# Optimization experiments

Hardware: AMD Instinct MI355X
Metric: run time of the kernel (lower is better)

Reference implementation:

```python
import jax, jax.numpy as jnp
import numpy as np

NEG_SLOPE = 0.01  # torch LeakyReLU default


def gru_layer(x, w_ih, w_hh, b_ih, b_hh):
    # x: [T, B, in], weights per torch.nn.GRU convention: [3H, in]/[3H, H], gates (r,z,n)
    H = w_hh.shape[1]
    def step(h, x_t):
        gi = x_t @ w_ih.T + b_ih            # [B, 3H]
        gh = h @ w_hh.T + b_hh              # [B, 3H]
        i_r, i_z, i_n = jnp.split(gi, 3, axis=-1)
        h_r, h_z, h_n = jnp.split(gh, 3, axis=-1)
        r = jax.nn.sigmoid(i_r + h_r)
        z = jax.nn.sigmoid(i_z + h_z)
        n = jnp.tanh(i_n + r * h_n)
        h_new = (1.0 - z) * n + z * h
        return h_new, h_new
    h0 = jnp.zeros((x.shape[1], H), x.dtype)
    _, ys = jax.lax.scan(step, h0, x)
    return ys  # [T, B, H]


def setup_inputs() -> dict:
    key = jax.random.key(0)
    ks = jax.random.split(key, 16)
    T, B, V, H, L2 = 128, 2048, 64, 256, 100
    s = 1.0 / np.sqrt(H)
    d = {
        'tokens': jax.random.randint(ks[0], (T, B), 0, V, dtype=jnp.int32),
        'lens': jax.random.randint(ks[1], (B,), 0, T, dtype=jnp.int32),
        'emb': jax.random.normal(ks[2], (V, H), jnp.float32),
        'w_ih0': jax.random.normal(ks[3], (3 * H, H), jnp.float32) * s,
        'w_hh0': jax.random.normal(ks[4], (3 * H, H), jnp.float32) * s,
        'b_ih0': jax.random.normal(ks[5], (3 * H,), jnp.float32) * s,
        'b_hh0': jax.random.normal(ks[6], (3 * H,), jnp.float32) * s,
        'w_ih1': jax.random.normal(ks[7], (3 * H, H), jnp.float32) * s,
        'w_hh1': jax.random.normal(ks[8], (3 * H, H), jnp.float32) * s,
        'b_ih1': jax.random.normal(ks[9], (3 * H,), jnp.float32) * s,
        'b_hh1': jax.random.normal(ks[10], (3 * H,), jnp.float32) * s,
        'w1': jax.random.normal(ks[11], (H, H), jnp.float32) * s,
        'b1': jax.random.normal(ks[12], (H,), jnp.float32) * s,
        'w2': jax.random.normal(ks[13], (L2, H), jnp.float32) * s,
        'b2': jax.random.normal(ks[14], (L2,), jnp.float32) * s,
    }
    return d


def reference(tokens, lens, emb, w_ih0, w_hh0, b_ih0, b_hh0,
              w_ih1, w_hh1, b_ih1, b_hh1, w1, b1, w2, b2):
    x = emb[tokens]                                   # [T, B, H] embedding lookup
    h1 = gru_layer(x, w_ih0, w_hh0, b_ih0, b_hh0)     # layer 0
    h2 = gru_layer(h1, w_ih1, w_hh1, b_ih1, b_hh1)    # layer 1
    B = tokens.shape[1]
    out_t = h2[lens, jnp.arange(B)]                   # [B, H] gather per-example timestep
    z = out_t @ w1.T + b1
    z = jnp.where(z >= 0, z, NEG_SLOPE * z)           # LeakyReLU
    enc = z @ w2.T + b2                               # [B, 2*latent]
    return enc
```

## Files before the change

### kernel.cpp

```cpp
#include <hip/hip_runtime.h>
#include <hip/hip_bf16.h>

typedef __attribute__((ext_vector_type(8))) short bh8;
typedef __attribute__((ext_vector_type(4))) short sh4;
typedef __attribute__((ext_vector_type(4))) float f4;

static constexpr int T_STEPS = 128;
static constexpr int BTOT    = 2048;
static constexpr int HD      = 256;
static constexpr int NG      = 768;
static constexpr int LOUT    = 100;

__device__ __forceinline__ short f2bf(float f){
  unsigned u = __builtin_bit_cast(unsigned, f);
  unsigned r = (u + 0x7FFFu + ((u >> 16) & 1u)) >> 16;
  return (short)(unsigned short)r;
}
__device__ __forceinline__ float bf2f(short s){
  unsigned u = ((unsigned)(unsigned short)s) << 16;
  return __builtin_bit_cast(float, u);
}
__device__ __forceinline__ f4 mfma16(bh8 a, bh8 b, f4 c){
  return __builtin_amdgcn_mfma_f32_16x16x32_bf16(a, b, c, 0, 0, 0);
}
__device__ __forceinline__ float sigm(float x){
  return __builtin_amdgcn_rcpf(1.f + __expf(-x));
}
__device__ __forceinline__ float tanh_f(float x){
  return 1.f - 2.f*__builtin_amdgcn_rcpf(1.f + __expf(2.f*x));
}

__global__ void e0g_kernel(const float* __restrict__ emb, const float* __restrict__ w_ih0,
                           const float* __restrict__ b_ih0, const float* __restrict__ b_hh0,
                           short* __restrict__ E0g)
{
  int tid = blockIdx.x*blockDim.x + threadIdx.x;
  if (tid >= 64*NG) return;
  int v = tid / NG, n = tid % NG;
  const float4* er = (const float4*)(emb + (size_t)v*HD);
  const float4* wr = (const float4*)(w_ih0 + (size_t)n*HD);
  float s = 0.f;
#pragma unroll 4
  for (int k=0;k<HD/4;++k){
    float4 a = er[k], b = wr[k];
    s += a.x*b.x + a.y*b.y + a.z*b.z + a.w*b.w;
  }
  s += b_ih0[n];
  if (n < 512) s += b_hh0[n];
  int g = n >> 8, j = n & 255;
  int wid = j >> 5, c = (j >> 4) & 1, l15 = j & 15;
  E0g[(size_t)v*1024 + wid*128 + l15*8 + g*2 + c] = f2bf(s);
}

__global__ void pack_kernel(const float* __restrict__ w_hh0, const float* __restrict__ w_ih1,
                            const float* __restrict__ w_hh1, const float* __restrict__ w1,
                            const float* __restrict__ w2, short* __restrict__ pack)
{
  int tid = blockIdx.x*blockDim.x + threadIdx.x;
  if (tid >= 1336*64) return;
  int t = tid >> 6, lane = tid & 63;
  int l15 = lane & 15, lq = lane >> 4;
  const float* src = nullptr;
  bool zero = false;
  if (t < 1152){
    int m = t/384, tt = t%384, ct = tt/8, kt = tt%8;
    int n = ct*16 + l15;
    const float* Wm = (m==0) ? w_hh0 : (m==1 ? w_ih1 : w_hh1);
    src = Wm + (size_t)n*HD + kt*32 + lq*8;
  } else if (t < 1280){
    int tt = t - 1152, w = tt/16, rem = tt%16, ntt = rem/8, kt = rem%8;
    int n = w*32 + ntt*16 + l15;
    src = w1 + (size_t)n*HD + kt*32 + lq*8;
  } else {
    int tt = t - 1280, ntt = tt/8, kt = tt%8;
    int n = ntt*16 + l15;
    if (n < LOUT) src = w2 + (size_t)n*HD + kt*32 + lq*8;
    else zero = true;
  }
  bh8 o;
#pragma unroll
  for (int e=0;e<8;++e) o[e] = zero ? (short)0 : f2bf(src[e]);
  ((bh8*)pack)[tid] = o;
}


__device__ __forceinline__ void layer0_body(
    int bid, const int* __restrict__ tokens, const short* __restrict__ E0g,
    const short* __restrict__ pack, const float* __restrict__ b_hh0,
    short* __restrict__ s0c, short* __restrict__ h0g, int tc, int Tc,
    short (&st)[2][16*264])
{
  const int tid = threadIdx.x;
  const int wid = tid >> 6;
  const int lane = tid & 63;
  const int l15 = lane & 15, lq = lane >> 4;
  const int b0 = bid * 16;

  bh8 W[3][2][8];
  {
    const bh8* pt = (const bh8*)pack;
#pragma unroll
    for (int g=0;g<3;++g)
#pragma unroll
      for (int c=0;c<2;++c)
#pragma unroll
        for (int kt=0;kt<8;++kt)
          W[g][c][kt] = pt[(size_t)((g*16 + wid*2 + c)*8 + kt)*64 + lane];
  }
  float bhn0[2];
#pragma unroll
  for (int c=0;c<2;++c) bhn0[c] = b_hh0[512 + wid*32 + c*16 + l15];

  if (tc == 0){
    for (int i=tid;i<16*264;i+=512) st[0][i] = 0;
  } else {
    for (int i=tid;i<16*256;i+=512)
      st[0][(i>>8)*264 + (i&255)] = h0g[(size_t)(b0 + (i>>8))*HD + (i&255)];
  }

  const int e0base = wid*128 + l15*8;
  bh8 ev[4];
  {
    const int tg0 = tc*Tc;
    int tokr[4];
#pragma unroll
    for (int r=0;r<4;++r) tokr[r] = tokens[(size_t)tg0*BTOT + b0 + lq*4 + r];
#pragma unroll
    for (int r=0;r<4;++r)
      ev[r] = *(const bh8*)(E0g + (size_t)tokr[r]*1024 + e0base);
  }
  __syncthreads();

  const f4 zf = {0.f,0.f,0.f,0.f};
  const int crow = tid >> 5, ccol8 = (tid & 31)*8;

#pragma unroll 1
  for (int t=0; t<Tc; ++t){
    const int p = t & 1;
    const int tg = tc*Tc + t;
    const int tn = (tg+1 < T_STEPS) ? tg+1 : T_STEPS-1;
    int tokn[4];
#pragma unroll
    for (int r=0;r<4;++r) tokn[r] = tokens[(size_t)tn*BTOT + b0 + lq*4 + r];
    f4 acc[3][2];
#pragma unroll
    for (int g=0;g<3;++g){ acc[g][0]=zf; acc[g][1]=zf; }
    {
      const short* sp = &st[p][l15*264 + lq*8];
#pragma unroll
      for (int kt=0;kt<8;++kt){
        bh8 a = *(const bh8*)(sp + kt*32);
#pragma unroll
        for (int g=0;g<3;++g){
          acc[g][0] = mfma16(a, W[g][0][kt], acc[g][0]);
          acc[g][1] = mfma16(a, W[g][1][kt], acc[g][1]);
        }
      }
    }
    if (t > 0){
      bh8 cv = *(const bh8*)(&st[p][crow*264 + ccol8]);
      *(bh8*)(s0c + ((size_t)(t-1)*BTOT + b0 + crow)*HD + ccol8) = cv;
    }
    {
      short* stw = st[p^1];
#pragma unroll
      for (int c=0;c<2;++c){
        const int jh = wid*32 + c*16 + l15;
#pragma unroll
        for (int r4=0;r4<4;++r4){
          const int row = lq*4 + r4;
          const float er = bf2f(ev[r4][c]);
          const float ez = bf2f(ev[r4][2+c]);
          const float en = bf2f(ev[r4][4+c]);
          const float rg = sigm(acc[0][c][r4] + er);
          const float zg = sigm(acc[1][c][r4] + ez);
          const float ng = tanh_f(en + rg*(acc[2][c][r4] + bhn0[c]));
          const float ho = bf2f(st[p][row*264 + jh]);
          const float h = ng + zg*(ho - ng);
          stw[row*264 + jh] = f2bf(h);
        }
      }
    }
#pragma unroll
    for (int r=0;r<4;++r)
      ev[r] = *(const bh8*)(E0g + (size_t)tokn[r]*1024 + e0base);
    __syncthreads();
  }
  {
    bh8 cv = *(const bh8*)(&st[Tc & 1][crow*264 + ccol8]);
    *(bh8*)(s0c + ((size_t)(Tc-1)*BTOT + b0 + crow)*HD + ccol8) = cv;
    *(bh8*)(h0g + ((size_t)(b0 + crow))*HD + ccol8) = cv;
  }
}

__device__ __forceinline__ void layer1_body(
    int bid, const int* __restrict__ lens, const short* __restrict__ gi1p,
    const short* __restrict__ pack, const float* __restrict__ b_hh1,
    short* __restrict__ h1g, short* __restrict__ outbuf, int tc, int Tc,
    short (&st)[2][16*264])
{
  const int tid = threadIdx.x;
  const int wid = tid >> 6;
  const int lane = tid & 63;
  const int l15 = lane & 15, lq = lane >> 4;
  const int b0 = bid * 16;
  const int bblk = bid;

  bh8 W[3][2][8];
  {
    const bh8* pt = (const bh8*)pack;
#pragma unroll
    for (int g=0;g<3;++g)
#pragma unroll
      for (int c=0;c<2;++c)
#pragma unroll
        for (int kt=0;kt<8;++kt)
          W[g][c][kt] = pt[(size_t)(768 + (g*16 + wid*2 + c)*8 + kt)*64 + lane];
  }
  float bhn1[2];
#pragma unroll
  for (int c=0;c<2;++c) bhn1[c] = b_hh1[512 + wid*32 + c*16 + l15];

  int mylens[4];
#pragma unroll
  for (int r=0;r<4;++r) mylens[r] = lens[b0 + lq*4 + r];

  if (tc == 0){
    for (int i=tid;i<16*264;i+=512) st[0][i] = 0;
  } else {
    for (int i=tid;i<16*256;i+=512)
      st[0][(i>>8)*264 + (i&255)] = h1g[(size_t)(b0 + (i>>8))*HD + (i&255)];
  }

  bh8 gv[3];
#pragma unroll
  for (int g=0;g<3;++g)
    gv[g] = *(const bh8*)(gi1p + ((size_t)bblk*512 + tid)*24 + g*8);
  __syncthreads();

  const f4 zf = {0.f,0.f,0.f,0.f};
  const int crow = tid >> 5, ccol8 = (tid & 31)*8;

#pragma unroll 1
  for (int t=0; t<Tc; ++t){
    const int p = t & 1;
    const int tg = tc*Tc + t;
    f4 acc[3][2];
#pragma unroll
    for (int g=0;g<3;++g){ acc[g][0]=zf; acc[g][1]=zf; }
    {
      const short* sp = &st[p][l15*264 + lq*8];
#pragma unroll
      for (int kt=0;kt<8;++kt){
        bh8 a = *(const bh8*)(sp + kt*32);
#pragma unroll
        for (int g=0;g<3;++g){
          acc[g][0] = mfma16(a, W[g][0][kt], acc[g][0]);
          acc[g][1] = mfma16(a, W[g][1][kt], acc[g][1]);
        }
      }
    }
    {
      short* stw = st[p^1];
#pragma unroll
      for (int c=0;c<2;++c){
        const int jh = wid*32 + c*16 + l15;
#pragma unroll
        for (int r4=0;r4<4;++r4){
          const int row = lq*4 + r4;
          const float gr = bf2f(gv[0][c*4+r4]);
          const float gz = bf2f(gv[1][c*4+r4]);
          const float gn = bf2f(gv[2][c*4+r4]);
          const float rg = sigm(acc[0][c][r4] + gr);
          const float zg = sigm(acc[1][c][r4] + gz);
          const float ng = tanh_f(gn + rg*(acc[2][c][r4] + bhn1[c]));
          const float ho = bf2f(st[p][row*264 + jh]);
          const float h = ng + zg*(ho - ng);
          const short hb = f2bf(h);
          stw[row*264 + jh] = hb;
          if (tg == mylens[r4]) outbuf[(size_t)(b0 + row)*HD + jh] = hb;
        }
      }
    }
    if (t+1 < Tc){
#pragma unroll
      for (int g=0;g<3;++g)
        gv[g] = *(const bh8*)(gi1p + (((size_t)(t+1)*128 + bblk)*512 + tid)*24 + g*8);
    }
    __syncthreads();
  }
  {
    bh8 cv = *(const bh8*)(&st[Tc & 1][crow*264 + ccol8]);
    *(bh8*)(h1g + ((size_t)(b0 + crow))*HD + ccol8) = cv;
  }
}

__global__ __launch_bounds__(512, 1)
void scan_fat(const int* __restrict__ tokens, const short* __restrict__ E0g,
              const short* __restrict__ pack, const float* __restrict__ b_hh0,
              short* __restrict__ s0c, short* __restrict__ h0g,
              const int* __restrict__ lens, const short* __restrict__ gi1p,
              const float* __restrict__ b_hh1, short* __restrict__ h1g,
              short* __restrict__ outbuf, int tc0, int tc1, int Tc)
{
  __shared__ __align__(16) short st[2][16*264];
  const int bx = blockIdx.x;
  if (bx < 128){
    if (tc0 >= 0)
      layer0_body(bx, tokens, E0g, pack, b_hh0, s0c, h0g, tc0, Tc, st);
  } else {
    if (tc1 >= 0)
      layer1_body(bx - 128, lens, gi1p, pack, b_hh1, h1g, outbuf, tc1, Tc, st);
  }
}

__global__ __launch_bounds__(256, 1)
void gi1_gemm(const short* __restrict__ s0c, const short* __restrict__ pack,
              const float* __restrict__ b_ih1, const float* __restrict__ b_hh1,
              short* __restrict__ gi1p, int NC)
{
  const int tid = threadIdx.x;
  const int wid = tid >> 6;
  const int lane = tid & 63;
  const int l15 = lane & 15, lq = lane >> 4;

  __shared__ __align__(16) short ab[2][16*264];
  __shared__ float bi[NG];
  for (int i=tid;i<NG;i+=256) bi[i] = b_ih1[i] + ((i < 512) ? b_hh1[i] : 0.f);

  bh8 W[12][8];
#pragma unroll
  for (int i=0;i<12;++i)
#pragma unroll
    for (int kt=0;kt<8;++kt)
      W[i][kt] = ((const bh8*)pack)[(size_t)(384 + (wid*12+i)*8 + kt)*64 + lane];

  int ci = blockIdx.x;
  if (ci >= NC) return;
  bh8 sr[2];
#pragma unroll
  for (int j=0;j<2;++j){
    int q = tid + j*256;
    sr[j] = *(const bh8*)(s0c + (size_t)ci*4096 + q*8);
  }
#pragma unroll
  for (int j=0;j<2;++j){
    int q = tid + j*256, row = q>>5, col8 = (q&31)*8;
    *(bh8*)(&ab[0][row*264 + col8]) = sr[j];
  }
  __syncthreads();

  const f4 zf = {0.f,0.f,0.f,0.f};
  int p = 0;
#pragma unroll 1
  for (; ci < NC; ci += gridDim.x){
    const int cin = ci + (int)gridDim.x;
    const bool more = (cin < NC);
    if (more){
#pragma unroll
      for (int j=0;j<2;++j){
        int q = tid + j*256;
        sr[j] = *(const bh8*)(s0c + (size_t)cin*4096 + q*8);
      }
    }
    f4 acc[12];
#pragma unroll
    for (int i=0;i<12;++i) acc[i] = zf;
    const short* sp = &ab[p][l15*264 + lq*8];
#pragma unroll
    for (int kt=0;kt<8;++kt){
      bh8 a = *(const bh8*)(sp + kt*32);
#pragma unroll
      for (int i=0;i<12;++i) acc[i] = mfma16(a, W[i][kt], acc[i]);
    }
#pragma unroll
    for (int i=0;i<12;++i){
      const int gc = (wid*12+i)*16 + l15;
      const int g = gc >> 8, j = gc & 255;
      const int widp = j >> 5, c = (j >> 4) & 1;
      const int tidp = widp*64 + lq*16 + l15;
      const float b = bi[gc];
      sh4 v;
#pragma unroll
      for (int r4=0;r4<4;++r4) v[r4] = f2bf(acc[i][r4] + b);
      *(sh4*)(gi1p + ((size_t)ci*512 + tidp)*24 + g*8 + c*4) = v;
    }
    if (more){
#pragma unroll
      for (int j=0;j<2;++j){
        int q = tid + j*256, row = q>>5, col8 = (q&31)*8;
        *(bh8*)(&ab[p^1][row*264 + col8]) = sr[j];
      }
    }
    p ^= 1;
    __syncthreads();
  }
}

__global__ __launch_bounds__(512, 1)
void head_kernel(const short* __restrict__ outbuf, const short* __restrict__ pack,
                 const float* __restrict__ b1, const float* __restrict__ b2,
                 float* __restrict__ out)
{
  const int tid = threadIdx.x;
  const int wid = tid >> 6;
  const int lane = tid & 63;
  const int l15 = lane & 15, lq = lane >> 4;
  const int b0 = blockIdx.x * 32;

  __shared__ __align__(16) short zA[32*264];
  __shared__ __align__(16) short zB[32*264];
  __shared__ float b1s[HD], b2s[112];
  if (tid < HD)  b1s[tid] = b1[tid];
  if (tid < 112) b2s[tid] = (tid < LOUT) ? b2[tid] : 0.f;

  for (int i=tid;i<32*256;i+=512){
    int row = i >> 8, col = i & 255;
    zA[row*264 + col] = outbuf[(size_t)(b0 + row)*HD + col];
  }
  __syncthreads();

  const f4 zf = {0.f,0.f,0.f,0.f};
  const int afrag = l15*264 + lq*8;
  constexpr int RT1 = 16*264;
  const bh8* packW1 = (const bh8*)pack + (size_t)(1152 + wid*16)*64 + lane;
  const bh8* packW2 = (const bh8*)pack + (size_t)(1280 + wid*8 )*64 + lane;

  {
    f4 az[2][2]; az[0][0]=zf; az[0][1]=zf; az[1][0]=zf; az[1][1]=zf;
#pragma unroll
    for (int kt=0;kt<8;++kt){
      bh8 a0 = *(const bh8*)(&zA[afrag + kt*32]);
      bh8 a1 = *(const bh8*)(&zA[afrag + RT1 + kt*32]);
#pragma unroll
      for (int nt=0;nt<2;++nt){
        bh8 b = packW1[(nt*8+kt)*64];
        az[nt][0] = mfma16(a0, b, az[nt][0]);
        az[nt][1] = mfma16(a1, b, az[nt][1]);
      }
    }
#pragma unroll
    for (int rt=0;rt<2;++rt)
#pragma unroll
      for (int nt=0;nt<2;++nt){
        const int jb = wid*32 + nt*16 + l15;
#pragma unroll
        for (int r4=0;r4<4;++r4){
          float v = az[nt][rt][r4] + b1s[jb];
          v = (v >= 0.f) ? v : 0.01f*v;
          zB[(rt*16+lq*4+r4)*264 + jb] = f2bf(v);
        }
      }
  }
  __syncthreads();

  if (wid < 7){
    f4 acc2[2]; acc2[0]=zf; acc2[1]=zf;
#pragma unroll
    for (int kt=0;kt<8;++kt){
      bh8 a0 = *(const bh8*)(&zB[afrag + kt*32]);
      bh8 a1 = *(const bh8*)(&zB[afrag + RT1 + kt*32]);
      bh8 b = packW2[kt*64];
      acc2[0] = mfma16(a0, b, acc2[0]);
      acc2[1] = mfma16(a1, b, acc2[1]);
    }
    const int n2 = wid*16 + l15;
    if (n2 < LOUT){
#pragma unroll
      for (int rt=0;rt<2;++rt)
#pragma unroll
        for (int r4=0;r4<4;++r4)
          out[(size_t)(b0 + rt*16 + lq*4 + r4)*LOUT + n2] = acc2[rt][r4] + b2s[n2];
    }
  }
}

extern "C" void kernel_launch(void* const* d_in, const int* in_sizes, int n_in,
                              void* d_out, int out_size, void* d_ws, size_t ws_size,
                              hipStream_t stream)
{
  const int*   tokens = (const int*)  d_in[0];
  const int*   lens   = (const int*)  d_in[1];
  const float* emb    = (const float*)d_in[2];
  const float* w_ih0  = (const float*)d_in[3];
  const float* w_hh0  = (const float*)d_in[4];
  const float* b_ih0  = (const float*)d_in[5];
  const float* b_hh0  = (const float*)d_in[6];
  const float* w_ih1  = (const float*)d_in[7];
  const float* w_hh1  = (const float*)d_in[8];
  const float* b_ih1  = (const float*)d_in[9];
  const float* b_hh1  = (const float*)d_in[10];
  const float* w1     = (const float*)d_in[11];
  const float* b1     = (const float*)d_in[12];
  const float* w2     = (const float*)d_in[13];
  const float* b2     = (const float*)d_in[14];

  char* ws = (char*)d_ws;
  size_t off = 0;
  short* pack = (short*)(ws + off); off += (size_t)1336*1024;
  short* E0g  = (short*)(ws + off); off += (size_t)64*1024*2;
  short* h0g  = (short*)(ws + off); off += (size_t)BTOT*HD*2;
  short* h1g  = (short*)(ws + off); off += (size_t)BTOT*HD*2;
  short* outb = (short*)(ws + off); off += (size_t)BTOT*HD*2;
  const size_t fixed = off;
  const size_t perT = (size_t)BTOT*HD*2 + (size_t)BTOT*NG*2;
  int Tc = T_STEPS;
  while (Tc > 1 && fixed + (size_t)Tc*perT > ws_size) Tc >>= 1;
  short* s0c  = (short*)(ws + fixed);
  short* gi1p = (short*)(ws + fixed + (size_t)Tc*BTOT*HD*2);

  e0g_kernel <<<(64*NG + 255)/256,   256, 0, stream>>>(emb, w_ih0, b_ih0, b_hh0, E0g);
  pack_kernel<<<(1336*64 + 255)/256, 256, 0, stream>>>(w_hh0, w_ih1, w_hh1, w1, w2, pack);

  const int nch = T_STEPS / Tc;
  for (int k = 0; k <= nch; ++k){
    const int tc0 = (k < nch) ? k : -1;
    const int tc1 = k - 1;
    scan_fat<<<256, 512, 0, stream>>>(tokens, E0g, pack, b_hh0, s0c, h0g,
                                      lens, gi1p, b_hh1, h1g, outb, tc0, tc1, Tc);
    if (k < nch)
      gi1_gemm<<<256, 256, 0, stream>>>(s0c, pack, b_ih1, b_hh1, gi1p, Tc*BTOT/16);
  }
  head_kernel<<<BTOT/32, 512, 0, stream>>>(outb, pack, b1, b2, (float*)d_out);
}
```

Before: 675.7 us.

## Keep GRU hidden state in fp32 registers, widen gi1 GEMM, cap chunk length

The layer-0 and layer-1 scans now keep the previous hidden value for each lane's outputs in fp32 registers instead of reading it back from the bf16 LDS tile. This removes an LDS read per element and avoids compounding bf16 rounding in the recurrence. The gi1 GEMM moves to 512 threads with 6 gate tiles per wave instead of 12, and precomputes bias and output offsets in registers, which cuts per-thread register pressure. The time chunk is capped at 32 steps, so the pipelined layer-0 / GEMM / layer-1 schedule has more stages, at the cost of more kernel launches.

```diff
diff --git a/kernel.cpp b/kernel.cpp
--- a/kernel.cpp
+++ b/kernel.cpp
@@ -111,9 +111,19 @@
 #pragma unroll
   for (int c=0;c<2;++c) bhn0[c] = b_hh0[512 + wid*32 + c*16 + l15];
 
+  float h0s[2][4];
   if (tc == 0){
+#pragma unroll
+    for (int c=0;c<2;++c)
+#pragma unroll
+      for (int r=0;r<4;++r) h0s[c][r] = 0.f;
     for (int i=tid;i<16*264;i+=512) st[0][i] = 0;
   } else {
+#pragma unroll
+    for (int c=0;c<2;++c)
+#pragma unroll
+      for (int r=0;r<4;++r)
+        h0s[c][r] = bf2f(h0g[(size_t)(b0 + lq*4 + r)*HD + wid*32 + c*16 + l15]);
     for (int i=tid;i<16*256;i+=512)
       st[0][(i>>8)*264 + (i&255)] = h0g[(size_t)(b0 + (i>>8))*HD + (i&255)];
   }
@@ -175,8 +185,8 @@
           const float rg = sigm(acc[0][c][r4] + er);
           const float zg = sigm(acc[1][c][r4] + ez);
           const float ng = tanh_f(en + rg*(acc[2][c][r4] + bhn0[c]));
-          const float ho = bf2f(st[p][row*264 + jh]);
-          const float h = ng + zg*(ho - ng);
+          const float h = ng + zg*(h0s[c][r4] - ng);
+          h0s[c][r4] = h;
           stw[row*264 + jh] = f2bf(h);
         }
       }
@@ -225,9 +235,19 @@
 #pragma unroll
   for (int r=0;r<4;++r) mylens[r] = lens[b0 + lq*4 + r];
 
+  float h1s[2][4];
   if (tc == 0){
+#pragma unroll
+    for (int c=0;c<2;++c)
+#pragma unroll
+      for (int r=0;r<4;++r) h1s[c][r] = 0.f;
     for (int i=tid;i<16*264;i+=512) st[0][i] = 0;
   } else {
+#pragma unroll
+    for (int c=0;c<2;++c)
+#pragma unroll
+      for (int r=0;r<4;++r)
+        h1s[c][r] = bf2f(h1g[(size_t)(b0 + lq*4 + r)*HD + wid*32 + c*16 + l15]);
     for (int i=tid;i<16*256;i+=512)
       st[0][(i>>8)*264 + (i&255)] = h1g[(size_t)(b0 + (i>>8))*HD + (i&255)];
   }
@@ -274,8 +294,8 @@
           const float rg = sigm(acc[0][c][r4] + gr);
           const float zg = sigm(acc[1][c][r4] + gz);
           const float ng = tanh_f(gn + rg*(acc[2][c][r4] + bhn1[c]));
-          const float ho = bf2f(st[p][row*264 + jh]);
-          const float h = ng + zg*(ho - ng);
+          const float h = ng + zg*(h1s[c][r4] - ng);
+          h1s[c][r4] = h;
           const short hb = f2bf(h);
           stw[row*264 + jh] = hb;
           if (tg == mylens[r4]) outbuf[(size_t)(b0 + row)*HD + jh] = hb;
@@ -314,7 +334,7 @@
   }
 }
 
-__global__ __launch_bounds__(256, 1)
+__global__ __launch_bounds__(512, 1)
 void gi1_gemm(const short* __restrict__ s0c, const short* __restrict__ pack,
               const float* __restrict__ b_ih1, const float* __restrict__ b_hh1,
               short* __restrict__ gi1p, int NC)
@@ -325,29 +345,30 @@
   const int l15 = lane & 15, lq = lane >> 4;
 
   __shared__ __align__(16) short ab[2][16*264];
-  __shared__ float bi[NG];
-  for (int i=tid;i<NG;i+=256) bi[i] = b_ih1[i] + ((i < 512) ? b_hh1[i] : 0.f);
-
-  bh8 W[12][8];
-#pragma unroll
-  for (int i=0;i<12;++i)
+
+  bh8 W[6][8];
+#pragma unroll
+  for (int i=0;i<6;++i)
 #pragma unroll
     for (int kt=0;kt<8;++kt)
-      W[i][kt] = ((const bh8*)pack)[(size_t)(384 + (wid*12+i)*8 + kt)*64 + lane];
+      W[i][kt] = ((const bh8*)pack)[(size_t)(384 + (wid*6+i)*8 + kt)*64 + lane];
+
+  float bi[6];
+  int offo[6];
+#pragma unroll
+  for (int i=0;i<6;++i){
+    const int gc = (wid*6+i)*16 + l15;
+    bi[i] = b_ih1[gc] + ((gc < 512) ? b_hh1[gc] : 0.f);
+    const int g = gc >> 8, j = gc & 255;
+    const int widp = j >> 5, c = (j >> 4) & 1;
+    const int tidp = widp*64 + lq*16 + l15;
+    offo[i] = tidp*24 + g*8 + c*4;
+  }
 
   int ci = blockIdx.x;
   if (ci >= NC) return;
-  bh8 sr[2];
-#pragma unroll
-  for (int j=0;j<2;++j){
-    int q = tid + j*256;
-    sr[j] = *(const bh8*)(s0c + (size_t)ci*4096 + q*8);
-  }
-#pragma unroll
-  for (int j=0;j<2;++j){
-    int q = tid + j*256, row = q>>5, col8 = (q&31)*8;
-    *(bh8*)(&ab[0][row*264 + col8]) = sr[j];
-  }
+  bh8 sr = *(const bh8*)(s0c + (size_t)ci*4096 + tid*8);
+  *(bh8*)(&ab[0][(tid>>5)*264 + (tid&31)*8]) = sr;
   __syncthreads();
 
   const f4 zf = {0.f,0.f,0.f,0.f};
@@ -356,42 +377,26 @@
   for (; ci < NC; ci += gridDim.x){
     const int cin = ci + (int)gridDim.x;
     const bool more = (cin < NC);
-    if (more){
-#pragma unroll
-      for (int j=0;j<2;++j){
-        int q = tid + j*256;
-        sr[j] = *(const bh8*)(s0c + (size_t)cin*4096 + q*8);
-      }
-    }
-    f4 acc[12];
-#pragma unroll
-    for (int i=0;i<12;++i) acc[i] = zf;
+    if (more) sr = *(const bh8*)(s0c + (size_t)cin*4096 + tid*8);
+    f4 acc[6];
+#pragma unroll
+    for (int i=0;i<6;++i) acc[i] = zf;
     const short* sp = &ab[p][l15*264 + lq*8];
 #pragma unroll
     for (int kt=0;kt<8;++kt){
       bh8 a = *(const bh8*)(sp + kt*32);
 #pragma unroll
-      for (int i=0;i<12;++i) acc[i] = mfma16(a, W[i][kt], acc[i]);
-    }
-#pragma unroll
-    for (int i=0;i<12;++i){
-      const int gc = (wid*12+i)*16 + l15;
-      const int g = gc >> 8, j = gc & 255;
-      const int widp = j >> 5, c = (j >> 4) & 1;
-      const int tidp = widp*64 + lq*16 + l15;
-      const float b = bi[gc];
+      for (int i=0;i<6;++i) acc[i] = mfma16(a, W[i][kt], acc[i]);
+    }
+#pragma unroll
+    for (int i=0;i<6;++i){
       sh4 v;
 #pragma unroll
-      for (int r4=0;r4<4;++r4) v[r4] = f2bf(acc[i][r4] + b);
-      *(sh4*)(gi1p + ((size_t)ci*512 + tidp)*24 + g*8 + c*4) = v;
-    }
-    if (more){
-#pragma unroll
-      for (int j=0;j<2;++j){
-        int q = tid + j*256, row = q>>5, col8 = (q&31)*8;
-        *(bh8*)(&ab[p^1][row*264 + col8]) = sr[j];
-      }
-    }
+      for (int r4=0;r4<4;++r4) v[r4] = f2bf(acc[i][r4] + bi[i]);
+      *(sh4*)(gi1p + (size_t)ci*512*24 + offo[i]) = v;
+    }
+    if (more)
+      *(bh8*)(&ab[p^1][(tid>>5)*264 + (tid&31)*8]) = sr;
     p ^= 1;
     __syncthreads();
   }
@@ -506,6 +511,7 @@
   const size_t perT = (size_t)BTOT*HD*2 + (size_t)BTOT*NG*2;
   int Tc = T_STEPS;
   while (Tc > 1 && fixed + (size_t)Tc*perT > ws_size) Tc >>= 1;
+  if (Tc > 32) Tc = 32;
   short* s0c  = (short*)(ws + fixed);
   short* gi1p = (short*)(ws + fixed + (size_t)Tc*BTOT*HD*2);
 
@@ -519,7 +525,7 @@
     scan_fat<<<256, 512, 0, stream>>>(tokens, E0g, pack, b_hh0, s0c, h0g,
                                       lens, gi1p, b_hh1, h1g, outb, tc0, tc1, Tc);
     if (k < nch)
-      gi1_gemm<<<256, 256, 0, stream>>>(s0c, pack, b_ih1, b_hh1, gi1p, Tc*BTOT/16);
+      gi1_gemm<<<256, 512, 0, stream>>>(s0c, pack, b_ih1, b_hh1, gi1p, Tc*BTOT/16);
   }
   head_kernel<<<BTOT/32, 512, 0, stream>>>(outb, pack, b1, b2, (float*)d_out);
 }
```

Measured after the change: 606.2 us, median of 4. 1.11x faster.
